# Optimization experiments

Hardware: AMD Instinct MI355X
Metric: run time of the kernel (lower is better)

## Reference

```python
import jax, jax.numpy as jnp
import numpy as np

SCALE = 20.0
EPS = 1e-8  # matches torch F.cosine_similarity eps


def _l2_normalize(x):
    # torch cosine_similarity clamps norms at eps
    norm = jnp.maximum(jnp.linalg.norm(x, axis=-1, keepdims=True), EPS)
    return x / norm


def setup_inputs() -> dict:
    key = jax.random.key(0)
    k1, k2 = jax.random.split(key)
    B, D = 4096, 1024
    anchor_emb = jax.random.normal(k1, (B, D), dtype=jnp.float32)
    pos_negs_emb = jax.random.normal(k2, (B, D), dtype=jnp.float32)
    return {"anchor_emb": anchor_emb, "pos_negs_emb": pos_negs_emb}


def reference(anchor_emb, pos_negs_emb):
    # cosine similarity as normalized GEMM (avoids (B,N,D) broadcast intermediate)
    a = _l2_normalize(anchor_emb)            # [B, D]
    p = _l2_normalize(pos_negs_emb)          # [N, D]
    scores = SCALE * jnp.einsum("bd,nd->bn", a, p)  # [B, N]
    B = scores.shape[0]
    # cross entropy with labels = arange(B): mean(logsumexp - diag)
    logZ = jax.scipy.special.logsumexp(scores, axis=1)  # [B]
    diag = scores[jnp.arange(B), jnp.arange(B)]          # [B]
    return jnp.mean(logZ - diag)
```

## Files before the change

### kernel.cpp

```cpp
#include <hip/hip_runtime.h>
#include <math.h>

#define NB 4096
#define ND 1024
#define SCALEF 20.0f
#define SQ 448.0f

typedef float floatx4 __attribute__((ext_vector_type(4)));
typedef int intx4 __attribute__((ext_vector_type(4)));

__device__ __forceinline__ void load16_to_lds(const void* g, void* l) {
    __builtin_amdgcn_global_load_lds(
        (const __attribute__((address_space(1))) void*)g,
        (__attribute__((address_space(3))) void*)l, 16, 0, 0);
}

__device__ __forceinline__ int q8(float x) {
    float c = fminf(fmaxf(x, -127.0f), 127.0f);
    return (int)rintf(c);
}

__global__ __launch_bounds__(256) void mnrl_norm_cvt(
    const float* __restrict__ A, const float* __restrict__ P,
    signed char* __restrict__ Aq, signed char* __restrict__ Pq,
    float* __restrict__ rowsum, float* __restrict__ out) {
    if (blockIdx.x == 0 && threadIdx.x == 0) out[0] = 0.0f;
    int row = blockIdx.x * 4 + (threadIdx.x >> 6);
    int lane = threadIdx.x & 63;
    bool is_a = row < NB;
    const float* src = is_a ? (A + (size_t)row * ND)
                            : (P + (size_t)(row - NB) * ND);
    unsigned int* dst = (unsigned int*)(is_a ? (Aq + (size_t)row * ND)
                                             : (Pq + (size_t)(row - NB) * ND));

    float4 v[4];
    float ss = 0.0f;
#pragma unroll
    for (int i = 0; i < 4; ++i) {
        v[i] = ((const float4*)src)[i * 64 + lane];
        ss += v[i].x * v[i].x + v[i].y * v[i].y + v[i].z * v[i].z + v[i].w * v[i].w;
    }
#pragma unroll
    for (int off = 32; off > 0; off >>= 1) ss += __shfl_xor(ss, off, 64);
    float inv = SQ / fmaxf(sqrtf(ss), 1e-8f);
#pragma unroll
    for (int i = 0; i < 4; ++i) {
        int q0 = q8(v[i].x * inv), q1 = q8(v[i].y * inv);
        int q2 = q8(v[i].z * inv), q3 = q8(v[i].w * inv);
        dst[i * 64 + lane] = (unsigned int)((q0 & 255) | ((q1 & 255) << 8) |
                                            ((q2 & 255) << 16) | (q3 << 24));
    }
    if (is_a && lane == 0) rowsum[row] = 0.0f;
}

__global__ __launch_bounds__(512, 2) void mnrl_gemm_lse(
    const signed char* __restrict__ Aq, const signed char* __restrict__ Pq,
    float* __restrict__ rowsum, float* __restrict__ diag) {
    __shared__ __align__(16) unsigned char lds_a[4][256 * 64];
    __shared__ __align__(16) unsigned char lds_b[4][256 * 64];

    int bid = blockIdx.x;
    int swz = (bid & 7) * 32 + (bid >> 3);
    int tile_m = swz >> 4;
    int tile_n = swz & 15;

    int t = threadIdx.x;
    int lane = t & 63;
    int w = t >> 6;
    int wm = w >> 2;
    int wn = w & 3;
    int quad = lane >> 4;
    int l16 = lane & 15;

    const signed char* Abase = Aq + (size_t)tile_m * 256 * ND;
    const signed char* Pbase = Pq + (size_t)tile_n * 256 * ND;

    int srow = lane >> 2;
    int chunk = (lane & 3) ^ ((lane >> 3) & 3);
    const signed char* srcA0 = Abase + (size_t)(w * 32 + srow) * ND + chunk * 16;
    const signed char* srcA1 = srcA0 + (size_t)16 * ND;
    const signed char* srcP0 = Pbase + (size_t)(w * 32 + srow) * ND + chunk * 16;
    const signed char* srcP1 = srcP0 + (size_t)16 * ND;
    const int dst0 = w * 2048;
    const int dst1 = w * 2048 + 1024;

    int key = (l16 >> 1) & 3;
    int slot16 = (quad ^ key) * 16;
    int offA[8], offB[4];
#pragma unroll
    for (int mt = 0; mt < 8; ++mt)
        offA[mt] = (wm * 128 + mt * 16 + l16) * 64 + slot16;
#pragma unroll
    for (int nt = 0; nt < 4; ++nt)
        offB[nt] = (wn * 64 + nt * 16 + l16) * 64 + slot16;

    intx4 acc[8][4];
#pragma unroll
    for (int mt = 0; mt < 8; ++mt)
#pragma unroll
        for (int nt = 0; nt < 4; ++nt) acc[mt][nt] = (intx4){0, 0, 0, 0};

#define STAGE(KT)                                                   \
    {                                                               \
        int koff_ = (KT) * 64;                                      \
        int b_ = (KT) & 3;                                          \
        load16_to_lds(srcA0 + koff_, &lds_a[b_][dst0]);             \
        load16_to_lds(srcA1 + koff_, &lds_a[b_][dst1]);             \
        load16_to_lds(srcP0 + koff_, &lds_b[b_][dst0]);             \
        load16_to_lds(srcP1 + koff_, &lds_b[b_][dst1]);             \
    }

#define K_BODY(KT, DOSTAGE)                                                  \
    {                                                                        \
        int b_ = (KT) & 3;                                                   \
        if (DOSTAGE) STAGE((KT) + 3);                                        \
        intx4 af[8], bv[4];                                                  \
        _Pragma("unroll") for (int mt = 0; mt < 8; ++mt)                     \
            af[mt] = *(const intx4*)&lds_a[b_][offA[mt]];                    \
        _Pragma("unroll") for (int nt = 0; nt < 4; ++nt)                     \
            bv[nt] = *(const intx4*)&lds_b[b_][offB[nt]];                    \
        __builtin_amdgcn_s_setprio(1);                                       \
        _Pragma("unroll") for (int mt = 0; mt < 8; ++mt)                     \
            _Pragma("unroll") for (int nt = 0; nt < 4; ++nt)                 \
                acc[mt][nt] = __builtin_amdgcn_mfma_i32_16x16x64_i8(         \
                    af[mt], bv[nt], acc[mt][nt], 0, 0, 0);                   \
        __builtin_amdgcn_s_setprio(0);                                       \
    }

    STAGE(0);
    STAGE(1);
    STAGE(2);

    for (int kt = 0; kt < 13; ++kt) {
        asm volatile("s_waitcnt vmcnt(8)" ::: "memory");
        __builtin_amdgcn_s_barrier();
        asm volatile("" ::: "memory");
        K_BODY(kt, 1);
    }
    asm volatile("s_waitcnt vmcnt(8)" ::: "memory");
    __builtin_amdgcn_s_barrier();
    asm volatile("" ::: "memory");
    K_BODY(13, 0);
    asm volatile("s_waitcnt vmcnt(4)" ::: "memory");
    __builtin_amdgcn_s_barrier();
    asm volatile("" ::: "memory");
    K_BODY(14, 0);
    asm volatile("s_waitcnt vmcnt(0)" ::: "memory");
    __builtin_amdgcn_s_barrier();
    asm volatile("" ::: "memory");
    K_BODY(15, 0);

#undef K_BODY
#undef STAGE

    const float SC = SCALEF / (SQ * SQ);
    bool diag_block = (tile_m == tile_n);
    float psum[8][4];
#pragma unroll
    for (int mt = 0; mt < 8; ++mt)
#pragma unroll
        for (int r = 0; r < 4; ++r) psum[mt][r] = 0.0f;

#pragma unroll
    for (int mt = 0; mt < 8; ++mt)
#pragma unroll
        for (int nt = 0; nt < 4; ++nt)
#pragma unroll
            for (int r = 0; r < 4; ++r) {
                float sc = SC * (float)acc[mt][nt][r];
                psum[mt][r] += __expf(sc - SCALEF);
                if (diag_block) {
                    int rt = wm * 128 + mt * 16 + quad * 4 + r;
                    int ct = wn * 64 + nt * 16 + l16;
                    if (rt == ct) diag[tile_m * 256 + rt] = sc;
                }
            }

    float* part = (float*)&lds_a[0][0];
#pragma unroll
    for (int mt = 0; mt < 8; ++mt)
#pragma unroll
        for (int r = 0; r < 4; ++r) {
            float v = psum[mt][r];
            v += __shfl_xor(v, 1, 64);
            v += __shfl_xor(v, 2, 64);
            v += __shfl_xor(v, 4, 64);
            v += __shfl_xor(v, 8, 64);
            if (l16 == 0) part[wn * 256 + wm * 128 + mt * 16 + quad * 4 + r] = v;
        }
    __syncthreads();
    if (t < 256) {
        float s = part[t] + part[256 + t] + part[512 + t] + part[768 + t];
        atomicAdd(&rowsum[tile_m * 256 + t], s);
    }
}

__global__ __launch_bounds__(256) void mnrl_finalize(const float* __restrict__ rowsum,
                                                     const float* __restrict__ diag,
                                                     float* __restrict__ out) {
    int t = threadIdx.x;
    int i = blockIdx.x * 256 + t;
    float local = (logf(rowsum[i]) + SCALEF) - diag[i];
#pragma unroll
    for (int off = 32; off > 0; off >>= 1) local += __shfl_down(local, off, 64);
    __shared__ float sred[4];
    if ((t & 63) == 0) sred[t >> 6] = local;
    __syncthreads();
    if (t == 0)
        atomicAdd(out, (sred[0] + sred[1] + sred[2] + sred[3]) * (1.0f / (float)NB));
}

extern "C" void kernel_launch(void* const* d_in, const int* in_sizes, int n_in,
                              void* d_out, int out_size, void* d_ws, size_t ws_size,
                              hipStream_t stream) {
    const float* A = (const float*)d_in[0];
    const float* P = (const float*)d_in[1];

    signed char* Aq = (signed char*)d_ws;
    signed char* Pq = Aq + (size_t)NB * ND;
    float* rowsum = (float*)(Pq + (size_t)NB * ND);
    float* diag = rowsum + NB;

    mnrl_norm_cvt<<<2 * NB / 4, 256, 0, stream>>>(A, P, Aq, Pq, rowsum,
                                                  (float*)d_out);
    mnrl_gemm_lse<<<16 * 16, 512, 0, stream>>>(Aq, Pq, rowsum, diag);
    mnrl_finalize<<<16, 256, 0, stream>>>(rowsum, diag, (float*)d_out);
}
```

Measured before the change: 100.1 us.

## Shrink GEMM tiles to 128x128 and fuse finalize via last-block counter

Moves the int8 GEMM+LSE kernel from 256x256 tiles with 512 threads and a 4-stage LDS pipeline to 128x128 tiles with 256 threads, double buffering and 4 blocks per CU. The grid grows from 256 to 1024 blocks, filling more CUs at the cost of more global reads per output. The separate finalize kernel is removed. Per-row-tile atomic counters let the last block of each row tile compute log-sum-exp minus diagonal and atomically add into the output. This saves a launch but adds fences and atomics and makes prefetch depth shallower.

Measured after the change: 167.9 us. 1.68x slower.

```diff
diff --git a/kernel.cpp b/kernel.cpp
--- a/kernel.cpp
+++ b/kernel.cpp
@@ -6,7 +6,6 @@
 #define SCALEF 20.0f
 #define SQ 448.0f
 
-typedef float floatx4 __attribute__((ext_vector_type(4)));
 typedef int intx4 __attribute__((ext_vector_type(4)));
 
 __device__ __forceinline__ void load16_to_lds(const void* g, void* l) {
@@ -23,8 +22,12 @@
 __global__ __launch_bounds__(256) void mnrl_norm_cvt(
     const float* __restrict__ A, const float* __restrict__ P,
     signed char* __restrict__ Aq, signed char* __restrict__ Pq,
-    float* __restrict__ rowsum, float* __restrict__ out) {
-    if (blockIdx.x == 0 && threadIdx.x == 0) out[0] = 0.0f;
+    float* __restrict__ rowsum, int* __restrict__ cnt,
+    float* __restrict__ out) {
+    if (blockIdx.x == 0) {
+        if (threadIdx.x == 0) out[0] = 0.0f;
+        if (threadIdx.x < 32) cnt[threadIdx.x] = 0;
+    }
     int row = blockIdx.x * 4 + (threadIdx.x >> 6);
     int lane = threadIdx.x & 63;
     bool is_a = row < NB;
@@ -53,27 +56,29 @@
     if (is_a && lane == 0) rowsum[row] = 0.0f;
 }
 
-__global__ __launch_bounds__(512, 2) void mnrl_gemm_lse(
+__global__ __launch_bounds__(256, 4) void mnrl_gemm_lse(
     const signed char* __restrict__ Aq, const signed char* __restrict__ Pq,
-    float* __restrict__ rowsum, float* __restrict__ diag) {
-    __shared__ __align__(16) unsigned char lds_a[4][256 * 64];
-    __shared__ __align__(16) unsigned char lds_b[4][256 * 64];
+    float* __restrict__ rowsum, float* __restrict__ diag,
+    int* __restrict__ cnt, float* __restrict__ out) {
+    __shared__ __align__(16) unsigned char lds_a[2][128 * 64];
+    __shared__ __align__(16) unsigned char lds_b[2][128 * 64];
+    __shared__ int is_last;
 
     int bid = blockIdx.x;
-    int swz = (bid & 7) * 32 + (bid >> 3);
-    int tile_m = swz >> 4;
-    int tile_n = swz & 15;
+    int swz = (bid & 7) * 128 + (bid >> 3);
+    int tile_m = swz >> 5;
+    int tile_n = swz & 31;
 
     int t = threadIdx.x;
     int lane = t & 63;
     int w = t >> 6;
-    int wm = w >> 2;
-    int wn = w & 3;
+    int wm = w >> 1;
+    int wn = w & 1;
     int quad = lane >> 4;
     int l16 = lane & 15;
 
-    const signed char* Abase = Aq + (size_t)tile_m * 256 * ND;
-    const signed char* Pbase = Pq + (size_t)tile_n * 256 * ND;
+    const signed char* Abase = Aq + (size_t)tile_m * 128 * ND;
+    const signed char* Pbase = Pq + (size_t)tile_n * 128 * ND;
 
     int srow = lane >> 2;
     int chunk = (lane & 3) ^ ((lane >> 3) & 3);
@@ -81,88 +86,66 @@
     const signed char* srcA1 = srcA0 + (size_t)16 * ND;
     const signed char* srcP0 = Pbase + (size_t)(w * 32 + srow) * ND + chunk * 16;
     const signed char* srcP1 = srcP0 + (size_t)16 * ND;
-    const int dst0 = w * 2048;
-    const int dst1 = w * 2048 + 1024;
-
-    int key = (l16 >> 1) & 3;
-    int slot16 = (quad ^ key) * 16;
-    int offA[8], offB[4];
-#pragma unroll
-    for (int mt = 0; mt < 8; ++mt)
-        offA[mt] = (wm * 128 + mt * 16 + l16) * 64 + slot16;
+
+    int slot16 = (quad ^ ((l16 >> 1) & 3)) * 16;
+    int offA[4], offB[4];
+#pragma unroll
+    for (int mt = 0; mt < 4; ++mt)
+        offA[mt] = (wm * 64 + mt * 16 + l16) * 64 + slot16;
 #pragma unroll
     for (int nt = 0; nt < 4; ++nt)
         offB[nt] = (wn * 64 + nt * 16 + l16) * 64 + slot16;
 
-    intx4 acc[8][4];
-#pragma unroll
-    for (int mt = 0; mt < 8; ++mt)
+    intx4 acc[4][4];
+#pragma unroll
+    for (int mt = 0; mt < 4; ++mt)
 #pragma unroll
         for (int nt = 0; nt < 4; ++nt) acc[mt][nt] = (intx4){0, 0, 0, 0};
 
 #define STAGE(KT)                                                   \
     {                                                               \
         int koff_ = (KT) * 64;                                      \
-        int b_ = (KT) & 3;                                          \
-        load16_to_lds(srcA0 + koff_, &lds_a[b_][dst0]);             \
-        load16_to_lds(srcA1 + koff_, &lds_a[b_][dst1]);             \
-        load16_to_lds(srcP0 + koff_, &lds_b[b_][dst0]);             \
-        load16_to_lds(srcP1 + koff_, &lds_b[b_][dst1]);             \
-    }
-
-#define K_BODY(KT, DOSTAGE)                                                  \
-    {                                                                        \
-        int b_ = (KT) & 3;                                                   \
-        if (DOSTAGE) STAGE((KT) + 3);                                        \
-        intx4 af[8], bv[4];                                                  \
-        _Pragma("unroll") for (int mt = 0; mt < 8; ++mt)                     \
-            af[mt] = *(const intx4*)&lds_a[b_][offA[mt]];                    \
-        _Pragma("unroll") for (int nt = 0; nt < 4; ++nt)                     \
-            bv[nt] = *(const intx4*)&lds_b[b_][offB[nt]];                    \
-        __builtin_amdgcn_s_setprio(1);                                       \
-        _Pragma("unroll") for (int mt = 0; mt < 8; ++mt)                     \
-            _Pragma("unroll") for (int nt = 0; nt < 4; ++nt)                 \
-                acc[mt][nt] = __builtin_amdgcn_mfma_i32_16x16x64_i8(         \
-                    af[mt], bv[nt], acc[mt][nt], 0, 0, 0);                   \
-        __builtin_amdgcn_s_setprio(0);                                       \
+        int b_ = (KT) & 1;                                          \
+        load16_to_lds(srcA0 + koff_, &lds_a[b_][w * 2048]);         \
+        load16_to_lds(srcA1 + koff_, &lds_a[b_][w * 2048 + 1024]);  \
+        load16_to_lds(srcP0 + koff_, &lds_b[b_][w * 2048]);         \
+        load16_to_lds(srcP1 + koff_, &lds_b[b_][w * 2048 + 1024]);  \
     }
 
     STAGE(0);
-    STAGE(1);
-    STAGE(2);
-
-    for (int kt = 0; kt < 13; ++kt) {
-        asm volatile("s_waitcnt vmcnt(8)" ::: "memory");
+
+    for (int kt = 0; kt < 16; ++kt) {
+        asm volatile("s_waitcnt vmcnt(0)" ::: "memory");
         __builtin_amdgcn_s_barrier();
         asm volatile("" ::: "memory");
-        K_BODY(kt, 1);
-    }
-    asm volatile("s_waitcnt vmcnt(8)" ::: "memory");
-    __builtin_amdgcn_s_barrier();
-    asm volatile("" ::: "memory");
-    K_BODY(13, 0);
-    asm volatile("s_waitcnt vmcnt(4)" ::: "memory");
-    __builtin_amdgcn_s_barrier();
-    asm volatile("" ::: "memory");
-    K_BODY(14, 0);
-    asm volatile("s_waitcnt vmcnt(0)" ::: "memory");
-    __builtin_amdgcn_s_barrier();
-    asm volatile("" ::: "memory");
-    K_BODY(15, 0);
-
-#undef K_BODY
+        if (kt < 15) STAGE(kt + 1);
+        const unsigned char* ba = &lds_a[kt & 1][0];
+        intx4 bv[4];
+#pragma unroll
+        for (int nt = 0; nt < 4; ++nt) bv[nt] = *(const intx4*)&lds_b[kt & 1][offB[nt]];
+        __builtin_amdgcn_s_setprio(1);
+#pragma unroll
+        for (int mt = 0; mt < 4; ++mt) {
+            intx4 av = *(const intx4*)&ba[offA[mt]];
+#pragma unroll
+            for (int nt = 0; nt < 4; ++nt)
+                acc[mt][nt] = __builtin_amdgcn_mfma_i32_16x16x64_i8(
+                    av, bv[nt], acc[mt][nt], 0, 0, 0);
+        }
+        __builtin_amdgcn_s_setprio(0);
+    }
 #undef STAGE
 
     const float SC = SCALEF / (SQ * SQ);
     bool diag_block = (tile_m == tile_n);
-    float psum[8][4];
-#pragma unroll
-    for (int mt = 0; mt < 8; ++mt)
+    float psum[4][4];
+#pragma unroll
+    for (int mt = 0; mt < 4; ++mt)
 #pragma unroll
         for (int r = 0; r < 4; ++r) psum[mt][r] = 0.0f;
 
 #pragma unroll
-    for (int mt = 0; mt < 8; ++mt)
+    for (int mt = 0; mt < 4; ++mt)
 #pragma unroll
         for (int nt = 0; nt < 4; ++nt)
 #pragma unroll
@@ -170,15 +153,18 @@
                 float sc = SC * (float)acc[mt][nt][r];
                 psum[mt][r] += __expf(sc - SCALEF);
                 if (diag_block) {
-                    int rt = wm * 128 + mt * 16 + quad * 4 + r;
+                    int rt = wm * 64 + mt * 16 + quad * 4 + r;
                     int ct = wn * 64 + nt * 16 + l16;
-                    if (rt == ct) diag[tile_m * 256 + rt] = sc;
+                    if (rt == ct)
+                        __hip_atomic_store(&diag[tile_m * 128 + rt], sc,
+                                           __ATOMIC_RELAXED,
+                                           __HIP_MEMORY_SCOPE_AGENT);
                 }
             }
 
     float* part = (float*)&lds_a[0][0];
 #pragma unroll
-    for (int mt = 0; mt < 8; ++mt)
+    for (int mt = 0; mt < 4; ++mt)
 #pragma unroll
         for (int r = 0; r < 4; ++r) {
             float v = psum[mt][r];
@@ -186,28 +172,40 @@
             v += __shfl_xor(v, 2, 64);
             v += __shfl_xor(v, 4, 64);
             v += __shfl_xor(v, 8, 64);
-            if (l16 == 0) part[wn * 256 + wm * 128 + mt * 16 + quad * 4 + r] = v;
+            if (l16 == 0) part[wn * 128 + wm * 64 + mt * 16 + quad * 4 + r] = v;
         }
     __syncthreads();
-    if (t < 256) {
-        float s = part[t] + part[256 + t] + part[512 + t] + part[768 + t];
-        atomicAdd(&rowsum[tile_m * 256 + t], s);
-    }
-}
-
-__global__ __launch_bounds__(256) void mnrl_finalize(const float* __restrict__ rowsum,
-                                                     const float* __restrict__ diag,
-                                                     float* __restrict__ out) {
-    int t = threadIdx.x;
-    int i = blockIdx.x * 256 + t;
-    float local = (logf(rowsum[i]) + SCALEF) - diag[i];
-#pragma unroll
-    for (int off = 32; off > 0; off >>= 1) local += __shfl_down(local, off, 64);
-    __shared__ float sred[4];
-    if ((t & 63) == 0) sred[t >> 6] = local;
+    if (t < 128) {
+        float s = part[t] + part[128 + t];
+        atomicAdd(&rowsum[tile_m * 128 + t], s);
+    }
+
+    __threadfence();
     __syncthreads();
-    if (t == 0)
-        atomicAdd(out, (sred[0] + sred[1] + sred[2] + sred[3]) * (1.0f / (float)NB));
+    if (t == 0) {
+        int old = __hip_atomic_fetch_add(&cnt[tile_m], 1, __ATOMIC_ACQ_REL,
+                                         __HIP_MEMORY_SCOPE_AGENT);
+        is_last = (old == 31);
+    }
+    __syncthreads();
+    if (is_last) {
+        __builtin_amdgcn_fence(__ATOMIC_ACQUIRE, "agent");
+        if (t < 128) {
+            int i = tile_m * 128 + t;
+            float rs = __hip_atomic_load(&rowsum[i], __ATOMIC_RELAXED,
+                                         __HIP_MEMORY_SCOPE_AGENT);
+            float dg = __hip_atomic_load(&diag[i], __ATOMIC_RELAXED,
+                                         __HIP_MEMORY_SCOPE_AGENT);
+            float local = (logf(rs) + SCALEF) - dg;
+            local += __shfl_xor(local, 1, 64);
+            local += __shfl_xor(local, 2, 64);
+            local += __shfl_xor(local, 4, 64);
+            local += __shfl_xor(local, 8, 64);
+            local += __shfl_xor(local, 16, 64);
+            local += __shfl_xor(local, 32, 64);
+            if ((t & 63) == 0) atomicAdd(out, local * (1.0f / (float)NB));
+        }
+    }
 }
 
 extern "C" void kernel_launch(void* const* d_in, const int* in_sizes, int n_in,
@@ -220,9 +218,10 @@
     signed char* Pq = Aq + (size_t)NB * ND;
     float* rowsum = (float*)(Pq + (size_t)NB * ND);
     float* diag = rowsum + NB;
-
-    mnrl_norm_cvt<<<2 * NB / 4, 256, 0, stream>>>(A, P, Aq, Pq, rowsum,
+    int* cnt = (int*)(diag + NB);
+
+    mnrl_norm_cvt<<<2 * NB / 4, 256, 0, stream>>>(A, P, Aq, Pq, rowsum, cnt,
                                                   (float*)d_out);
-    mnrl_gemm_lse<<<16 * 16, 512, 0, stream>>>(Aq, Pq, rowsum, diag);
-    mnrl_finalize<<<16, 256, 0, stream>>>(rowsum, diag, (float*)d_out);
-}
+    mnrl_gemm_lse<<<32 * 32, 256, 0, stream>>>(Aq, Pq, rowsum, diag, cnt,
+                                               (float*)d_out);
+}
```
